# Performance work log

Hardware: AMD Instinct MI355X
Metric: run time of the kernel (lower is better)

Reference implementation:

```python
import jax, jax.numpy as jnp
import numpy as np


def setup_inputs() -> dict:
    key = jax.random.key(0)
    ks = jax.random.split(key, 10)
    N, S, H = 500000, 128, 64
    s = lambda k, shape, fan_in: jax.random.normal(k, shape, dtype=jnp.float32) / np.sqrt(fan_in)
    return {
        "my_state": jax.random.normal(ks[0], (S,), dtype=jnp.float32),
        "neighbor_states": jax.random.normal(ks[1], (N, S), dtype=jnp.float32),
        "embed_w": s(ks[2], (S, H), S),
        "embed_b": s(ks[3], (H,), S),
        "key_w": s(ks[4], (H, H), H),
        "key_b": s(ks[5], (H,), H),
        "query_w": s(ks[6], (S + H, H), S + H),
        "query_b": s(ks[7], (H,), S + H),
        "attn_w": s(ks[8], (2 * H, 1), 2 * H),
        "attn_b": s(ks[9], (1,), 2 * H),
    }


def reference(my_state, neighbor_states, embed_w, embed_b, key_w, key_b,
              query_w, query_b, attn_w, attn_b):
    H = embed_w.shape[1]
    # per-neighbor embeddings and keys: [N, H]
    emb = neighbor_states @ embed_w + embed_b
    keys = emb @ key_w + key_b
    # query from own state + mean neighbor embedding: [H]
    mean_emb = emb.mean(axis=0)
    query = jnp.concatenate([my_state, mean_emb], axis=-1) @ query_w + query_b
    # attention_net(cat(query, key)) split so we never materialize [N, 2H]
    wq, wk = attn_w[:H, 0], attn_w[H:, 0]
    scores = keys @ wk + (query @ wq + attn_b[0])  # [N]
    attention_weights = jax.nn.softmax(scores, axis=0)  # [N]
    weighted_embedding = attention_weights @ emb  # [H]
    return weighted_embedding, attention_weights
```

## Files before the change

### kernel.cpp

```cpp
#include <hip/hip_runtime.h>
#include <math.h>


#define S_DIM 128
#define H_DIM 64
#define NBLK  2048

__global__ void k_precompute_u(const float* __restrict__ embed_w,
                               const float* __restrict__ key_w,
                               const float* __restrict__ attn_w,
                               float* __restrict__ u)
{
    __shared__ float kv[H_DIM];
    const int t = threadIdx.x;
    if (t < H_DIM) {
        float acc = 0.f;
        #pragma unroll 8
        for (int j = 0; j < H_DIM; ++j) acc += key_w[t * H_DIM + j] * attn_w[H_DIM + j];
        kv[t] = acc;
    }
    __syncthreads();
    float acc = 0.f;
    #pragma unroll 8
    for (int h = 0; h < H_DIM; ++h) acc += embed_w[t * H_DIM + h] * kv[h];
    u[t] = acc;
}

__global__ __launch_bounds__(256) void k_pass1(
    const float* __restrict__ X,
    const float* __restrict__ u,
    float* __restrict__ scores_out,
    float* __restrict__ pm,
    float* __restrict__ pz,
    float* __restrict__ pt_t,
    int N)
{
    const int lane = threadIdx.x & 63;
    const int li   = lane & 31;
    const int half = lane >> 5;
    const int w    = threadIdx.x >> 6;
    const int gw   = blockIdx.x * 4 + w;
    const int W    = NBLK * 4;
    const int pairs = (N + 1) >> 1;

    const float4 u4 = *(const float4*)(u + 4 * li);

    float  m = -1e30f, Z = 0.f;
    float4 t = make_float4(0.f, 0.f, 0.f, 0.f);

    int pr = gw;
    float4 x = make_float4(0.f, 0.f, 0.f, 0.f);
    if (pr < pairs) {
        const int row  = 2 * pr + half;
        const int rowc = row < N ? row : N - 1;
        x = *(const float4*)(X + (size_t)rowc * S_DIM + 4 * li);
    }

    while (pr < pairs) {
        const int npr = pr + W;
        float4 xn;
        if (npr < pairs) {
            const int row  = 2 * npr + half;
            const int rowc = row < N ? row : N - 1;
            xn = *(const float4*)(X + (size_t)rowc * S_DIM + 4 * li);
        }

        float p = x.x * u4.x + x.y * u4.y + x.z * u4.z + x.w * u4.w;
        p += __shfl_xor(p, 1);
        p += __shfl_xor(p, 2);
        p += __shfl_xor(p, 4);
        p += __shfl_xor(p, 8);
        p += __shfl_xor(p, 16);

        const int   row = 2 * pr + half;
        const float s   = (row < N) ? p : -INFINITY;
        if (li == 0 && row < N) scores_out[row] = s;

        const float mn = fmaxf(m, s);
        const float rs = __expf(m - mn);
        const float e  = __expf(s - mn);
        Z   = Z * rs + e;
        t.x = t.x * rs + e * x.x;
        t.y = t.y * rs + e * x.y;
        t.z = t.z * rs + e * x.z;
        t.w = t.w * rs + e * x.w;
        m   = mn;

        x = xn; pr = npr;
    }

    __shared__ float sT[8][S_DIM];
    __shared__ float sm[8], sZ[8];
    const int hs = w * 2 + half;
    sT[hs][4 * li + 0] = t.x;
    sT[hs][4 * li + 1] = t.y;
    sT[hs][4 * li + 2] = t.z;
    sT[hs][4 * li + 3] = t.w;
    if (li == 0) { sm[hs] = m; sZ[hs] = Z; }
    __syncthreads();

    float mb = sm[0];
    #pragma unroll
    for (int h = 1; h < 8; ++h) mb = fmaxf(mb, sm[h]);

    const int k = threadIdx.x;
    if (k < S_DIM) {
        float acc = 0.f;
        #pragma unroll
        for (int h = 0; h < 8; ++h) acc += sT[h][k] * __expf(sm[h] - mb);
        pt_t[(size_t)k * NBLK + blockIdx.x] = acc;
    }
    if (k == 0) {
        float Zb = 0.f;
        #pragma unroll
        for (int h = 0; h < 8; ++h) Zb += sZ[h] * __expf(sm[h] - mb);
        pm[blockIdx.x] = mb;
        pz[blockIdx.x] = Zb;
    }
}

__global__ __launch_bounds__(256) void k_pass2(
    const float* __restrict__ pm, const float* __restrict__ pz,
    const float* __restrict__ pt_t,
    float* __restrict__ tS,
    float* __restrict__ mz)
{
    const int k   = blockIdx.x;
    const int tid = threadIdx.x;
    __shared__ float red[256];

    float m = -1e30f;
    for (int b = tid; b < NBLK; b += 256) m = fmaxf(m, pm[b]);
    red[tid] = m; __syncthreads();
    for (int s = 128; s; s >>= 1) { if (tid < s) red[tid] = fmaxf(red[tid], red[tid + s]); __syncthreads(); }
    const float mstar = red[0]; __syncthreads();

    float z = 0.f, tacc = 0.f;
    for (int b = tid; b < NBLK; b += 256) {
        const float sc = __expf(pm[b] - mstar);
        z    += pz[b] * sc;
        tacc += pt_t[(size_t)k * NBLK + b] * sc;
    }
    red[tid] = z; __syncthreads();
    for (int s = 128; s; s >>= 1) { if (tid < s) red[tid] += red[tid + s]; __syncthreads(); }
    const float Zstar = red[0]; __syncthreads();

    red[tid] = tacc; __syncthreads();
    for (int s = 128; s; s >>= 1) { if (tid < s) red[tid] += red[tid + s]; __syncthreads(); }
    if (tid == 0) {
        tS[k] = red[0] / Zstar;
        if (k == 0) { mz[0] = mstar; mz[1] = Zstar; }
    }
}

__global__ void k_emb(const float* __restrict__ tS, const float* __restrict__ embed_w,
                      const float* __restrict__ embed_b, float* __restrict__ out_emb)
{
    const int h = threadIdx.x;
    float acc = embed_b[h];
    #pragma unroll 8
    for (int k = 0; k < S_DIM; ++k) acc += tS[k] * embed_w[k * H_DIM + h];
    out_emb[h] = acc;
}

__global__ __launch_bounds__(256) void k_pass3(
    float* __restrict__ sw, const float* __restrict__ mz, int N)
{
    const float mstar = mz[0];
    const float invZ  = 1.0f / mz[1];
    const int n4 = N >> 2;
    const int stride = gridDim.x * blockDim.x;
    for (int i = blockIdx.x * blockDim.x + threadIdx.x; i < n4; i += stride) {
        float4 v = ((float4*)sw)[i];
        v.x = __expf(v.x - mstar) * invZ;
        v.y = __expf(v.y - mstar) * invZ;
        v.z = __expf(v.z - mstar) * invZ;
        v.w = __expf(v.w - mstar) * invZ;
        ((float4*)sw)[i] = v;
    }
    if (blockIdx.x == 0 && threadIdx.x == 0) {
        for (int i = n4 << 2; i < N; ++i) sw[i] = __expf(sw[i] - mstar) * invZ;
    }
}

extern "C" void kernel_launch(void* const* d_in, const int* in_sizes, int n_in,
                              void* d_out, int out_size, void* d_ws, size_t ws_size,
                              hipStream_t stream) {
    const float* X       = (const float*)d_in[1];
    const float* embed_w = (const float*)d_in[2];
    const float* embed_b = (const float*)d_in[3];
    const float* key_w   = (const float*)d_in[4];
    const float* attn_w  = (const float*)d_in[8];
    float* out = (float*)d_out;

    const int N = in_sizes[1] / S_DIM;

    float* ws   = (float*)d_ws;
    float* u    = ws;
    float* mz   = ws + 128;
    float* tS   = ws + 192;
    float* pm   = ws + 512;
    float* pz   = pm + NBLK;
    float* pt_t = pz + NBLK;

    float* out_emb = out;
    float* out_w   = out + H_DIM;

    k_precompute_u<<<1, 128, 0, stream>>>(embed_w, key_w, attn_w, u);
    k_pass1<<<NBLK, 256, 0, stream>>>(X, u, out_w, pm, pz, pt_t, N);
    k_pass2<<<S_DIM, 256, 0, stream>>>(pm, pz, pt_t, tS, mz);
    k_emb<<<1, H_DIM, 0, stream>>>(tS, embed_w, embed_b, out_emb);
    k_pass3<<<((N >> 2) + 255) / 256, 256, 0, stream>>>(out_w, mz, N);
}
```

Baseline: 65.67 us.

## Fuse u precompute into pass1, merge emb into pass3, dual-stream pass1 loop

Removes the single-block u-precompute kernel by having every pass1 block recompute the folded key/attention vector in shared memory. It also folds the output-embedding kernel into block 0 of pass3, cutting launches from five to three. Pass1 now handles two rows per half-wave per iteration with two independent online-softmax accumulators, merged at the end, to raise memory-level parallelism. The cost is redundant per-block compute of u (about 16K FMAs and reads of key_w and embed_w in every one of 2048 blocks) plus extra registers.

```diff
diff --git a/kernel.cpp b/kernel.cpp
--- a/kernel.cpp
+++ b/kernel.cpp
@@ -6,76 +6,71 @@
 #define H_DIM 64
 #define NBLK  2048
 
-__global__ void k_precompute_u(const float* __restrict__ embed_w,
-                               const float* __restrict__ key_w,
-                               const float* __restrict__ attn_w,
-                               float* __restrict__ u)
-{
-    __shared__ float kv[H_DIM];
-    const int t = threadIdx.x;
-    if (t < H_DIM) {
-        float acc = 0.f;
-        #pragma unroll 8
-        for (int j = 0; j < H_DIM; ++j) acc += key_w[t * H_DIM + j] * attn_w[H_DIM + j];
-        kv[t] = acc;
-    }
-    __syncthreads();
-    float acc = 0.f;
-    #pragma unroll 8
-    for (int h = 0; h < H_DIM; ++h) acc += embed_w[t * H_DIM + h] * kv[h];
-    u[t] = acc;
-}
-
 __global__ __launch_bounds__(256) void k_pass1(
     const float* __restrict__ X,
-    const float* __restrict__ u,
+    const float* __restrict__ embed_w,
+    const float* __restrict__ key_w,
+    const float* __restrict__ attn_w,
     float* __restrict__ scores_out,
     float* __restrict__ pm,
     float* __restrict__ pz,
     float* __restrict__ pt_t,
     int N)
 {
-    const int lane = threadIdx.x & 63;
+    __shared__ float s_kv[H_DIM];
+    __shared__ float s_u[S_DIM];
+    __shared__ float sT[8][S_DIM];
+    __shared__ float sm[8], sZ[8];
+
+    const int tid  = threadIdx.x;
+    const int lane = tid & 63;
     const int li   = lane & 31;
     const int half = lane >> 5;
-    const int w    = threadIdx.x >> 6;
-    const int gw   = blockIdx.x * 4 + w;
-    const int W    = NBLK * 4;
+    const int w    = tid >> 6;
+
+    if (tid < H_DIM) {
+        float acc = 0.f;
+        #pragma unroll 8
+        for (int j = 0; j < H_DIM; ++j) acc += key_w[tid * H_DIM + j] * attn_w[H_DIM + j];
+        s_kv[tid] = acc;
+    }
+    __syncthreads();
+    if (tid < S_DIM) {
+        float acc = 0.f;
+        #pragma unroll 8
+        for (int h = 0; h < H_DIM; ++h) acc += embed_w[tid * H_DIM + h] * s_kv[h];
+        s_u[tid] = acc;
+    }
+    __syncthreads();
+
+    const float4 u4 = *(const float4*)(s_u + 4 * li);
+
+    const int gw    = blockIdx.x * 4 + w;
+    const int W     = NBLK * 4;
+    const int P2    = 2 * W;
     const int pairs = (N + 1) >> 1;
 
-    const float4 u4 = *(const float4*)(u + 4 * li);
-
-    float  m = -1e30f, Z = 0.f;
-    float4 t = make_float4(0.f, 0.f, 0.f, 0.f);
-
-    int pr = gw;
-    float4 x = make_float4(0.f, 0.f, 0.f, 0.f);
-    if (pr < pairs) {
-        const int row  = 2 * pr + half;
+    auto loadp = [&](int p) -> float4 {
+        const int row  = 2 * p + half;
         const int rowc = row < N ? row : N - 1;
-        x = *(const float4*)(X + (size_t)rowc * S_DIM + 4 * li);
-    }
-
-    while (pr < pairs) {
-        const int npr = pr + W;
-        float4 xn;
-        if (npr < pairs) {
-            const int row  = 2 * npr + half;
-            const int rowc = row < N ? row : N - 1;
-            xn = *(const float4*)(X + (size_t)rowc * S_DIM + 4 * li);
-        }
-
-        float p = x.x * u4.x + x.y * u4.y + x.z * u4.z + x.w * u4.w;
-        p += __shfl_xor(p, 1);
-        p += __shfl_xor(p, 2);
-        p += __shfl_xor(p, 4);
-        p += __shfl_xor(p, 8);
-        p += __shfl_xor(p, 16);
-
-        const int   row = 2 * pr + half;
-        const float s   = (row < N) ? p : -INFINITY;
-        if (li == 0 && row < N) scores_out[row] = s;
-
+        return *(const float4*)(X + (size_t)rowc * S_DIM + 4 * li);
+    };
+
+    float  ma = -1e30f, Za = 0.f, mb_ = -1e30f, Zb_ = 0.f;
+    float4 ta = make_float4(0.f, 0.f, 0.f, 0.f);
+    float4 tb = make_float4(0.f, 0.f, 0.f, 0.f);
+
+    auto proc = [&](const float4& x, int p, float& m, float& Z, float4& t) {
+        float pp = x.x * u4.x + x.y * u4.y + x.z * u4.z + x.w * u4.w;
+        pp += __shfl_xor(pp, 1);
+        pp += __shfl_xor(pp, 2);
+        pp += __shfl_xor(pp, 4);
+        pp += __shfl_xor(pp, 8);
+        pp += __shfl_xor(pp, 16);
+        const int  row = 2 * p + half;
+        const bool v   = row < N;
+        if (li == 0 && v) scores_out[row] = pp;
+        const float s  = v ? pp : -INFINITY;
         const float mn = fmaxf(m, s);
         const float rs = __expf(m - mn);
         const float e  = __expf(s - mn);
@@ -84,37 +79,54 @@
         t.y = t.y * rs + e * x.y;
         t.z = t.z * rs + e * x.z;
         t.w = t.w * rs + e * x.w;
-        m   = mn;
-
-        x = xn; pr = npr;
-    }
-
-    __shared__ float sT[8][S_DIM];
-    __shared__ float sm[8], sZ[8];
+        m = mn;
+    };
+
+    int pr = gw;
+    float4 xa = loadp(pr);
+    float4 xb = loadp(pr + W);
+
+    while (pr < pairs) {
+        const int nx = pr + P2;
+        float4 na = xa, nb = xb;
+        if (nx < pairs) {
+            na = loadp(nx);
+            nb = loadp(nx + W);
+        }
+        proc(xa, pr,     ma,  Za,  ta);
+        proc(xb, pr + W, mb_, Zb_, tb);
+        xa = na; xb = nb; pr = nx;
+    }
+
+    const float mm = fmaxf(ma, mb_);
+    const float ra = __expf(ma - mm), rb = __expf(mb_ - mm);
+    float  Zh = Za * ra + Zb_ * rb;
+    float4 th = make_float4(ta.x * ra + tb.x * rb, ta.y * ra + tb.y * rb,
+                            ta.z * ra + tb.z * rb, ta.w * ra + tb.w * rb);
+
     const int hs = w * 2 + half;
-    sT[hs][4 * li + 0] = t.x;
-    sT[hs][4 * li + 1] = t.y;
-    sT[hs][4 * li + 2] = t.z;
-    sT[hs][4 * li + 3] = t.w;
-    if (li == 0) { sm[hs] = m; sZ[hs] = Z; }
+    sT[hs][4 * li + 0] = th.x;
+    sT[hs][4 * li + 1] = th.y;
+    sT[hs][4 * li + 2] = th.z;
+    sT[hs][4 * li + 3] = th.w;
+    if (li == 0) { sm[hs] = mm; sZ[hs] = Zh; }
     __syncthreads();
 
-    float mb = sm[0];
+    float mbk = sm[0];
     #pragma unroll
-    for (int h = 1; h < 8; ++h) mb = fmaxf(mb, sm[h]);
-
-    const int k = threadIdx.x;
-    if (k < S_DIM) {
+    for (int h = 1; h < 8; ++h) mbk = fmaxf(mbk, sm[h]);
+
+    if (tid < S_DIM) {
         float acc = 0.f;
         #pragma unroll
-        for (int h = 0; h < 8; ++h) acc += sT[h][k] * __expf(sm[h] - mb);
-        pt_t[(size_t)k * NBLK + blockIdx.x] = acc;
-    }
-    if (k == 0) {
+        for (int h = 0; h < 8; ++h) acc += sT[h][tid] * __expf(sm[h] - mbk);
+        pt_t[(size_t)tid * NBLK + blockIdx.x] = acc;
+    }
+    if (tid == 0) {
         float Zb = 0.f;
         #pragma unroll
-        for (int h = 0; h < 8; ++h) Zb += sZ[h] * __expf(sm[h] - mb);
-        pm[blockIdx.x] = mb;
+        for (int h = 0; h < 8; ++h) Zb += sZ[h] * __expf(sm[h] - mbk);
+        pm[blockIdx.x] = mbk;
         pz[blockIdx.x] = Zb;
     }
 }
@@ -153,33 +165,36 @@
     }
 }
 
-__global__ void k_emb(const float* __restrict__ tS, const float* __restrict__ embed_w,
-                      const float* __restrict__ embed_b, float* __restrict__ out_emb)
+__global__ __launch_bounds__(256) void k_pass3(
+    float* __restrict__ sw, const float* __restrict__ mz,
+    const float* __restrict__ tS, const float* __restrict__ embed_w,
+    const float* __restrict__ embed_b, float* __restrict__ out_emb, int N)
 {
-    const int h = threadIdx.x;
-    float acc = embed_b[h];
-    #pragma unroll 8
-    for (int k = 0; k < S_DIM; ++k) acc += tS[k] * embed_w[k * H_DIM + h];
-    out_emb[h] = acc;
-}
-
-__global__ __launch_bounds__(256) void k_pass3(
-    float* __restrict__ sw, const float* __restrict__ mz, int N)
-{
+    const int tid = threadIdx.x;
+    if (blockIdx.x == 0) {
+        if (tid < H_DIM) {
+            float acc = embed_b[tid];
+            #pragma unroll 8
+            for (int k = 0; k < S_DIM; ++k) acc += tS[k] * embed_w[k * H_DIM + tid];
+            out_emb[tid] = acc;
+        } else if (tid == H_DIM) {
+            const float mstar = mz[0];
+            const float invZ  = 1.0f / mz[1];
+            for (int i = (N >> 2) << 2; i < N; ++i) sw[i] = __expf(sw[i] - mstar) * invZ;
+        }
+        return;
+    }
     const float mstar = mz[0];
     const float invZ  = 1.0f / mz[1];
     const int n4 = N >> 2;
-    const int stride = gridDim.x * blockDim.x;
-    for (int i = blockIdx.x * blockDim.x + threadIdx.x; i < n4; i += stride) {
+    const int stride = (gridDim.x - 1) * 256;
+    for (int i = (blockIdx.x - 1) * 256 + tid; i < n4; i += stride) {
         float4 v = ((float4*)sw)[i];
         v.x = __expf(v.x - mstar) * invZ;
         v.y = __expf(v.y - mstar) * invZ;
         v.z = __expf(v.z - mstar) * invZ;
         v.w = __expf(v.w - mstar) * invZ;
         ((float4*)sw)[i] = v;
-    }
-    if (blockIdx.x == 0 && threadIdx.x == 0) {
-        for (int i = n4 << 2; i < N; ++i) sw[i] = __expf(sw[i] - mstar) * invZ;
     }
 }
 
@@ -196,19 +211,17 @@
     const int N = in_sizes[1] / S_DIM;
 
     float* ws   = (float*)d_ws;
-    float* u    = ws;
-    float* mz   = ws + 128;
-    float* tS   = ws + 192;
-    float* pm   = ws + 512;
+    float* mz   = ws;
+    float* tS   = ws + 64;
+    float* pm   = ws + 256;
     float* pz   = pm + NBLK;
     float* pt_t = pz + NBLK;
 
     float* out_emb = out;
     float* out_w   = out + H_DIM;
 
-    k_precompute_u<<<1, 128, 0, stream>>>(embed_w, key_w, attn_w, u);
-    k_pass1<<<NBLK, 256, 0, stream>>>(X, u, out_w, pm, pz, pt_t, N);
+    k_pass1<<<NBLK, 256, 0, stream>>>(X, embed_w, key_w, attn_w, out_w, pm, pz, pt_t, N);
     k_pass2<<<S_DIM, 256, 0, stream>>>(pm, pz, pt_t, tS, mz);
-    k_emb<<<1, H_DIM, 0, stream>>>(tS, embed_w, embed_b, out_emb);
-    k_pass3<<<((N >> 2) + 255) / 256, 256, 0, stream>>>(out_w, mz, N);
-}
+    const int nb3 = ((N >> 2) + 255) / 256 + 1;
+    k_pass3<<<nb3, 256, 0, stream>>>(out_w, mz, tS, embed_w, embed_b, out_emb, N);
+}
```

New measurement: 70.81 us. 7.8% more time.
